# Kernel optimization log

Hardware: AMD Instinct MI355X
Metric: run time of the kernel (lower is better)

Reference implementation:

```python
import jax, jax.numpy as jnp
import numpy as np

N = 50000
E = 800000
G = 16  # graphs in batch
NEG_SLOPE = 0.2


def gatv2_layer(x, src, dst, Wl, bl, Wr, br, att, bias, concat):
    # PyG GATv2Conv: x_j = lin_l(x)[src], x_i = lin_r(x)[dst]
    H, C = att.shape
    n = x.shape[0]
    xl = (x @ Wl + bl).reshape(n, H, C)  # source transform
    xr = (x @ Wr + br).reshape(n, H, C)  # target transform
    e = jax.nn.leaky_relu(xl[src] + xr[dst], NEG_SLOPE)  # [E,H,C]
    score = jnp.einsum('ehc,hc->eh', e, att)             # [E,H]
    # segment softmax over incoming edges of each dst node
    smax = jax.ops.segment_max(score, dst, num_segments=n)   # [n,H]
    ex = jnp.exp(score - smax[dst])
    denom = jax.ops.segment_sum(ex, dst, num_segments=n)
    alpha = ex / (denom[dst] + 1e-16)                        # [E,H]
    out = jax.ops.segment_sum(alpha[:, :, None] * xl[src], dst, num_segments=n)  # [n,H,C]
    if concat:
        return out.reshape(n, H * C) + bias
    return out.mean(axis=1) + bias


def setup_inputs() -> dict:
    key = jax.random.key(0)
    ks = jax.random.split(key, 20)
    x = jax.random.normal(ks[0], (N, 8), dtype=jnp.float32)
    edge_index = jax.random.randint(ks[1], (2, E), 0, N, dtype=jnp.int64)
    batch = jnp.sort(jax.random.randint(ks[2], (N,), 0, G, dtype=jnp.int64))

    def glorot(k, shape):
        lim = np.sqrt(6.0 / (shape[0] + shape[1]))
        return jax.random.uniform(k, shape, jnp.float32, -lim, lim)

    params = dict(
        Wl1=glorot(ks[3], (8, 128)), bl1=jnp.zeros((128,), jnp.float32),
        Wr1=glorot(ks[4], (8, 128)), br1=jnp.zeros((128,), jnp.float32),
        att1=glorot(ks[5], (2, 64)), b1=jnp.zeros((128,), jnp.float32),
        Wl2=glorot(ks[6], (128, 128)), bl2=jnp.zeros((128,), jnp.float32),
        Wr2=glorot(ks[7], (128, 128)), br2=jnp.zeros((128,), jnp.float32),
        att2=glorot(ks[8], (2, 64)), b2=jnp.zeros((128,), jnp.float32),
        Wl3=glorot(ks[9], (128, 32)), bl3=jnp.zeros((32,), jnp.float32),
        Wr3=glorot(ks[10], (128, 32)), br3=jnp.zeros((32,), jnp.float32),
        att3=glorot(ks[11], (1, 32)), b3=jnp.zeros((32,), jnp.float32),
    )
    return dict(x=x, edge_index=edge_index, batch=batch, **params)


def reference(x, edge_index, batch,
              Wl1, bl1, Wr1, br1, att1, b1,
              Wl2, bl2, Wr2, br2, att2, b2,
              Wl3, bl3, Wr3, br3, att3, b3):
    n = x.shape[0]
    loops = jnp.arange(n, dtype=edge_index.dtype)
    src = jnp.concatenate([edge_index[0], loops])  # add_self_loops=True (PyG default)
    dst = jnp.concatenate([edge_index[1], loops])

    h = gatv2_layer(x, src, dst, Wl1, bl1, Wr1, br1, att1, b1, concat=True)
    h = jax.nn.elu(h)
    # dropout(p=0.5) is identity in eval mode
    h = gatv2_layer(h, src, dst, Wl2, bl2, Wr2, br2, att2, b2, concat=True)
    h = jax.nn.elu(h)
    h = gatv2_layer(h, src, dst, Wl3, bl3, Wr3, br3, att3, b3, concat=False)
    h = jax.nn.elu(h)  # [n,32]

    counts = jax.ops.segment_sum(jnp.ones((n,), h.dtype), batch, num_segments=G)
    pooled_mean = jax.ops.segment_sum(h, batch, num_segments=G) / counts[:, None]
    pooled_max = jax.ops.segment_max(h, batch, num_segments=G)
    return jnp.concatenate([pooled_mean, pooled_max], axis=1)  # [G,64]
```

## Files before the change

kernel.cpp:

```cpp
#include <hip/hip_runtime.h>
#include <hip/hip_bf16.h>
#include <math.h>


__device__ __forceinline__ float lrelu(float x) { return x > 0.f ? x : 0.2f * x; }
__device__ __forceinline__ float elu1(float x) { return x > 0.f ? x : expm1f(x); }

__device__ __forceinline__ unsigned f2ord(float x) {
    unsigned b = __float_as_uint(x);
    return (b & 0x80000000u) ? ~b : (b | 0x80000000u);
}
__device__ __forceinline__ float ord2f(unsigned u) {
    unsigned b = (u & 0x80000000u) ? (u & 0x7FFFFFFFu) : ~u;
    return __uint_as_float(b);
}
__device__ __forceinline__ unsigned short f2bf(float f) {
    unsigned u = __float_as_uint(f);
    unsigned r = u + 0x7FFFu + ((u >> 16) & 1u);
    return (unsigned short)(r >> 16);
}

__global__ void k_zero_i32(int* __restrict__ p, int n) {
    int i = blockIdx.x * blockDim.x + threadIdx.x;
    if (i < n) p[i] = 0;
}

__global__ void k_hist(const int* __restrict__ ei, int E, int N, int* __restrict__ deg) {
    int e = blockIdx.x * blockDim.x + threadIdx.x;
    int Etot = E + N;
    if (e >= Etot) return;
    int d = (e < E) ? ei[E + e] : (e - E);
    atomicAdd(&deg[d], 1);
}

__global__ void __launch_bounds__(1024) k_scan(const int* __restrict__ deg, int n,
                                               int* __restrict__ row_off, int* __restrict__ cursor) {
    __shared__ int wsum[16];
    __shared__ int sbase;
    int tid = threadIdx.x;
    int lane = tid & 63, w = tid >> 6;
    if (tid == 0) sbase = 0;
    __syncthreads();
    for (int start = 0; start < n; start += 1024) {
        int i = start + tid;
        int v = (i < n) ? deg[i] : 0;
        int s = v;
        #pragma unroll
        for (int d = 1; d < 64; d <<= 1) {
            int t = __shfl_up(s, d, 64);
            if (lane >= d) s += t;
        }
        if (lane == 63) wsum[w] = s;
        __syncthreads();
        int wbase = 0;
        for (int k = 0; k < w; k++) wbase += wsum[k];
        int excl = sbase + wbase + (s - v);
        if (i < n) { row_off[i] = excl; cursor[i] = excl; }
        __syncthreads();
        if (tid == 1023) sbase = excl + v;
        __syncthreads();
    }
    if (tid == 0) row_off[n] = sbase;
}

__global__ void k_scatter(const int* __restrict__ ei, int E, int N,
                          int* __restrict__ cursor,
                          int* __restrict__ csr_src) {
    int e = blockIdx.x * blockDim.x + threadIdx.x;
    int Etot = E + N;
    if (e >= Etot) return;
    int s, d;
    if (e < E) { s = ei[e]; d = ei[E + e]; } else { s = e - E; d = e - E; }
    int p = atomicAdd(&cursor[d], 1);
    csr_src[p] = s;
}

template <int K>
__global__ void k_linear2b(const float* __restrict__ x, int N,
                           const float* __restrict__ Wl, const float* __restrict__ bl,
                           const float* __restrict__ Wr, const float* __restrict__ br,
                           unsigned short* __restrict__ xlb, float* __restrict__ xr) {
    constexpr int MH = 128, NCG = 64;
    __shared__ float xs[32 * K];
    int tid = threadIdx.x;
    int node0 = blockIdx.x * 32;
    for (int idx = tid * 4; idx < 32 * K; idx += NCG * 4 * 4) {
        int node = node0 + idx / K;
        float4 v = make_float4(0.f, 0.f, 0.f, 0.f);
        if (node < N) v = *(const float4*)(x + (size_t)node0 * K + idx);
        *(float4*)(xs + idx) = v;
    }
    __syncthreads();

    int cg = tid % NCG;
    int ng = tid / NCG;
    bool rightSide = cg >= (MH / 4);
    int c = (rightSide ? cg - MH / 4 : cg) * 4;
    const float* W  = rightSide ? Wr : Wl;
    const float* bb = rightSide ? br : bl;

    float acc[8][4];
    #pragma unroll
    for (int i = 0; i < 8; i++)
        #pragma unroll
        for (int j = 0; j < 4; j++) acc[i][j] = 0.f;

    const float* xrow = xs + ng * 8 * K;
    for (int k0 = 0; k0 < K; k0 += 4) {
        float4 wv[4];
        #pragma unroll
        for (int kk = 0; kk < 4; kk++)
            wv[kk] = *(const float4*)(W + (size_t)(k0 + kk) * MH + c);
        #pragma unroll
        for (int i = 0; i < 8; i++) {
            float4 xv = *(const float4*)(xrow + i * K + k0);
            float xvk[4] = {xv.x, xv.y, xv.z, xv.w};
            #pragma unroll
            for (int kk = 0; kk < 4; kk++) {
                acc[i][0] += xvk[kk] * wv[kk].x;
                acc[i][1] += xvk[kk] * wv[kk].y;
                acc[i][2] += xvk[kk] * wv[kk].z;
                acc[i][3] += xvk[kk] * wv[kk].w;
            }
        }
    }
    float4 bv = *(const float4*)(bb + c);
    #pragma unroll
    for (int i = 0; i < 8; i++) {
        int node = node0 + ng * 8 + i;
        if (node >= N) continue;
        float o0 = acc[i][0] + bv.x, o1 = acc[i][1] + bv.y;
        float o2 = acc[i][2] + bv.z, o3 = acc[i][3] + bv.w;
        if (rightSide) {
            *(float4*)(xr + (size_t)node * MH + c) = make_float4(o0, o1, o2, o3);
        } else {
            ushort4 ub = make_ushort4(f2bf(o0), f2bf(o1), f2bf(o2), f2bf(o3));
            *(ushort4*)(xlb + (size_t)node * MH + c) = ub;
        }
    }
}

__global__ void __launch_bounds__(256) k_linear3(
        const float* __restrict__ x, int N,
        const float* __restrict__ Wl, const float* __restrict__ bl,
        const float* __restrict__ Wr, const float* __restrict__ br,
        float* __restrict__ xl, float* __restrict__ xr) {
    __shared__ float xs[32 * 128];
    int tid = threadIdx.x;
    int node0 = blockIdx.x * 32;
    for (int idx = tid * 4; idx < 32 * 128; idx += 256 * 4) {
        int node = node0 + idx / 128;
        float4 v = make_float4(0.f, 0.f, 0.f, 0.f);
        if (node < N) v = *(const float4*)(x + (size_t)node0 * 128 + idx);
        *(float4*)(xs + idx) = v;
    }
    __syncthreads();
    int cg = tid & 15, ng = tid >> 4;
    bool rightSide = cg >= 8;
    int c = (rightSide ? cg - 8 : cg) * 4;
    const float* W  = rightSide ? Wr : Wl;
    const float* bb = rightSide ? br : bl;
    float* out      = rightSide ? xr : xl;

    float acc[2][4];
    #pragma unroll
    for (int i = 0; i < 2; i++)
        #pragma unroll
        for (int j = 0; j < 4; j++) acc[i][j] = 0.f;

    const float* xrow = xs + ng * 2 * 128;
    for (int k0 = 0; k0 < 128; k0 += 4) {
        float4 wv[4];
        #pragma unroll
        for (int kk = 0; kk < 4; kk++)
            wv[kk] = *(const float4*)(W + (size_t)(k0 + kk) * 32 + c);
        #pragma unroll
        for (int i = 0; i < 2; i++) {
            float4 xv = *(const float4*)(xrow + i * 128 + k0);
            float xvk[4] = {xv.x, xv.y, xv.z, xv.w};
            #pragma unroll
            for (int kk = 0; kk < 4; kk++) {
                acc[i][0] += xvk[kk] * wv[kk].x;
                acc[i][1] += xvk[kk] * wv[kk].y;
                acc[i][2] += xvk[kk] * wv[kk].z;
                acc[i][3] += xvk[kk] * wv[kk].w;
            }
        }
    }
    float4 bv = *(const float4*)(bb + c);
    #pragma unroll
    for (int i = 0; i < 2; i++) {
        int node = node0 + ng * 2 + i;
        if (node < N) {
            float4 o = make_float4(acc[i][0] + bv.x, acc[i][1] + bv.y,
                                   acc[i][2] + bv.z, acc[i][3] + bv.w);
            *(float4*)(out + (size_t)node * 32 + c) = o;
        }
    }
}

__global__ void k_fusedb(const int* __restrict__ row_off, const int* __restrict__ csr_src,
                         const unsigned short* __restrict__ xlb, const float* __restrict__ xr,
                         const float* __restrict__ att, const float* __restrict__ bias,
                         float* __restrict__ hout, int N) {
    constexpr int HC = 128, CPL = 8, GROUP = 8;
    int wid = (blockIdx.x * blockDim.x + threadIdx.x) >> 6;
    int lane = threadIdx.x & 63;
    if (wid >= N) return;
    int slot = lane >> 4;
    int j = lane & 15;
    int c0 = j * CPL;

    int p0 = row_off[wid], p1 = row_off[wid + 1];

    float xrv[CPL], attv[CPL];
    {
        float4 a = *(const float4*)(xr + (size_t)wid * HC + c0);
        float4 b = *(const float4*)(xr + (size_t)wid * HC + c0 + 4);
        xrv[0] = a.x; xrv[1] = a.y; xrv[2] = a.z; xrv[3] = a.w;
        xrv[4] = b.x; xrv[5] = b.y; xrv[6] = b.z; xrv[7] = b.w;
        float4 c = *(const float4*)(att + c0);
        float4 d = *(const float4*)(att + c0 + 4);
        attv[0] = c.x; attv[1] = c.y; attv[2] = c.z; attv[3] = c.w;
        attv[4] = d.x; attv[5] = d.y; attv[6] = d.z; attv[7] = d.w;
    }

    float m = -INFINITY, den = 0.f;
    float acc[CPL];
    #pragma unroll
    for (int q = 0; q < CPL; q++) acc[q] = 0.f;

    int p = p0 + slot;
    int s = (p < p1) ? csr_src[p] : 0;
    while (p < p1) {
        int pn = p + 4;
        int sn = (pn < p1) ? csr_src[pn] : 0;
        int4 rv = *(const int4*)(xlb + (size_t)s * HC + c0);
        float xlv[CPL];
        {
            unsigned u0 = (unsigned)rv.x, u1 = (unsigned)rv.y;
            unsigned u2 = (unsigned)rv.z, u3 = (unsigned)rv.w;
            xlv[0] = __uint_as_float(u0 << 16); xlv[1] = __uint_as_float(u0 & 0xFFFF0000u);
            xlv[2] = __uint_as_float(u1 << 16); xlv[3] = __uint_as_float(u1 & 0xFFFF0000u);
            xlv[4] = __uint_as_float(u2 << 16); xlv[5] = __uint_as_float(u2 & 0xFFFF0000u);
            xlv[6] = __uint_as_float(u3 << 16); xlv[7] = __uint_as_float(u3 & 0xFFFF0000u);
        }
        float part = 0.f;
        #pragma unroll
        for (int q = 0; q < CPL; q++) {
            float t = xlv[q] + xrv[q];
            part = fmaf(fmaxf(t, 0.2f * t), attv[q], part);
        }
        #pragma unroll
        for (int msk = 1; msk < GROUP; msk <<= 1) part += __shfl_xor(part, msk, 64);
        if (part > m + 8.f) {
            float corr = __expf(m - part);
            den *= corr;
            #pragma unroll
            for (int q = 0; q < CPL; q++) acc[q] *= corr;
            m = part;
        }
        float ex = __expf(part - m);
        den += ex;
        #pragma unroll
        for (int q = 0; q < CPL; q++) acc[q] = fmaf(ex, xlv[q], acc[q]);
        p = pn; s = sn;
    }
    float mAll = fmaxf(m, __shfl_xor(m, 16, 64));
    mAll = fmaxf(mAll, __shfl_xor(mAll, 32, 64));
    float scale = __expf(m - mAll);
    float dtot = den * scale;
    dtot += __shfl_xor(dtot, 16, 64);
    dtot += __shfl_xor(dtot, 32, 64);
    #pragma unroll
    for (int q = 0; q < CPL; q++) {
        float a = acc[q] * scale;
        a += __shfl_xor(a, 16, 64);
        a += __shfl_xor(a, 32, 64);
        acc[q] = a;
    }
    if (slot == 0) {
        float inv = 1.0f / (dtot + 1e-16f);
        #pragma unroll
        for (int q = 0; q < CPL; q++) {
            float v = acc[q] * inv + bias[c0 + q];
            hout[(size_t)wid * HC + c0 + q] = elu1(v);
        }
    }
}

template <int CPL>
__device__ __forceinline__ void loadrow(const float* __restrict__ p, float* v) {
    if constexpr (CPL == 8) {
        float4 a = ((const float4*)p)[0];
        float4 b = ((const float4*)p)[1];
        v[0] = a.x; v[1] = a.y; v[2] = a.z; v[3] = a.w;
        v[4] = b.x; v[5] = b.y; v[6] = b.z; v[7] = b.w;
    } else {
        float2 a = ((const float2*)p)[0];
        v[0] = a.x; v[1] = a.y;
    }
}

template <int HC, int C>
__global__ void k_fused(const int* __restrict__ row_off, const int* __restrict__ csr_src,
                        const float* __restrict__ xl, const float* __restrict__ xr,
                        const float* __restrict__ att, const float* __restrict__ bias,
                        float* __restrict__ hout, int N) {
    constexpr int CPL = HC / 16;
    constexpr int GROUP = (16 * C) / HC;
    int wid = (blockIdx.x * blockDim.x + threadIdx.x) >> 6;
    int lane = threadIdx.x & 63;
    if (wid >= N) return;
    int slot = lane >> 4;
    int j = lane & 15;
    int c0 = j * CPL;

    int p0 = row_off[wid], p1 = row_off[wid + 1];

    float xrv[CPL], attv[CPL];
    loadrow<CPL>(xr + (size_t)wid * HC + c0, xrv);
    loadrow<CPL>(att + c0, attv);

    float m = -INFINITY, den = 0.f;
    float acc[CPL];
    #pragma unroll
    for (int q = 0; q < CPL; q++) acc[q] = 0.f;

    int p = p0 + slot;
    int s = (p < p1) ? csr_src[p] : 0;
    while (p < p1) {
        int pn = p + 4;
        int sn = (pn < p1) ? csr_src[pn] : 0;
        float xlv[CPL];
        loadrow<CPL>(xl + (size_t)s * HC + c0, xlv);
        float part = 0.f;
        #pragma unroll
        for (int q = 0; q < CPL; q++) {
            float t = xlv[q] + xrv[q];
            part = fmaf(fmaxf(t, 0.2f * t), attv[q], part);
        }
        #pragma unroll
        for (int msk = 1; msk < GROUP; msk <<= 1) part += __shfl_xor(part, msk, 64);
        if (part > m + 8.f) {
            float corr = __expf(m - part);
            den *= corr;
            #pragma unroll
            for (int q = 0; q < CPL; q++) acc[q] *= corr;
            m = part;
        }
        float ex = __expf(part - m);
        den += ex;
        #pragma unroll
        for (int q = 0; q < CPL; q++) acc[q] = fmaf(ex, xlv[q], acc[q]);
        p = pn; s = sn;
    }
    float mAll = fmaxf(m, __shfl_xor(m, 16, 64));
    mAll = fmaxf(mAll, __shfl_xor(mAll, 32, 64));
    float scale = __expf(m - mAll);
    float dtot = den * scale;
    dtot += __shfl_xor(dtot, 16, 64);
    dtot += __shfl_xor(dtot, 32, 64);
    #pragma unroll
    for (int q = 0; q < CPL; q++) {
        float a = acc[q] * scale;
        a += __shfl_xor(a, 16, 64);
        a += __shfl_xor(a, 32, 64);
        acc[q] = a;
    }
    if (slot == 0) {
        float inv = 1.0f / (dtot + 1e-16f);
        #pragma unroll
        for (int q = 0; q < CPL; q++) {
            float v = acc[q] * inv + bias[c0 + q];
            hout[(size_t)wid * HC + c0 + q] = elu1(v);
        }
    }
}

__global__ void __launch_bounds__(256) k_pool_partial(
        const float* __restrict__ h, const int* __restrict__ batch, int N, int G,
        float* __restrict__ gsum, unsigned* __restrict__ gmax) {
    __shared__ float lsum[512];
    __shared__ unsigned lmax[512];
    int tid = threadIdx.x;
    for (int i = tid; i < G * 32; i += 256) { lsum[i] = 0.f; lmax[i] = 0u; }
    __syncthreads();
    int chunk = (N + gridDim.x - 1) / gridDim.x;
    int start = blockIdx.x * chunk;
    int end = min(N, start + chunk);
    int col = tid & 31, row = tid >> 5;
    int gc = -1; float ps = 0.f; unsigned pm = 0u;
    for (int i = start + row; i < end; i += 8) {
        int g = batch[i];
        if (g != gc) {
            if (gc >= 0) { atomicAdd(&lsum[gc * 32 + col], ps); atomicMax(&lmax[gc * 32 + col], pm); }
            gc = g; ps = 0.f; pm = 0u;
        }
        float v = h[(size_t)i * 32 + col];
        ps += v; pm = max(pm, f2ord(v));
    }
    if (gc >= 0) { atomicAdd(&lsum[gc * 32 + col], ps); atomicMax(&lmax[gc * 32 + col], pm); }
    __syncthreads();
    for (int i = tid; i < G * 32; i += 256) {
        if (lmax[i]) {
            atomicAdd(&gsum[i], lsum[i]);
            atomicMax(&gmax[i], lmax[i]);
        }
    }
}

__global__ void k_pool_final(const float* __restrict__ gsum, const unsigned* __restrict__ gmax,
                             const int* __restrict__ batch, int N, float* __restrict__ out) {
    int g = blockIdx.x;
    int t = threadIdx.x;
    __shared__ int s_cnt;
    if (t == 0) {
        int lo = 0, hi = N;
        while (lo < hi) { int m = (lo + hi) >> 1; if (batch[m] < g) lo = m + 1; else hi = m; }
        int a = lo;
        lo = a; hi = N;
        while (lo < hi) { int m = (lo + hi) >> 1; if (batch[m] < g + 1) lo = m + 1; else hi = m; }
        s_cnt = lo - a;
    }
    __syncthreads();
    if (t < 32) {
        out[g * 64 + t] = gsum[g * 32 + t] / (float)max(s_cnt, 1);
    } else {
        out[g * 64 + t] = ord2f(gmax[g * 32 + (t - 32)]);
    }
}

extern "C" void kernel_launch(void* const* d_in, const int* in_sizes, int n_in,
                              void* d_out, int out_size, void* d_ws, size_t ws_size,
                              hipStream_t stream) {
    const float* x      = (const float*)d_in[0];
    const int*   ei     = (const int*)d_in[1];
    const int*   batch  = (const int*)d_in[2];
    const float* Wl1 = (const float*)d_in[3],  *bl1 = (const float*)d_in[4];
    const float* Wr1 = (const float*)d_in[5],  *br1 = (const float*)d_in[6];
    const float* att1= (const float*)d_in[7],  *b1  = (const float*)d_in[8];
    const float* Wl2 = (const float*)d_in[9],  *bl2 = (const float*)d_in[10];
    const float* Wr2 = (const float*)d_in[11], *br2 = (const float*)d_in[12];
    const float* att2= (const float*)d_in[13], *b2  = (const float*)d_in[14];
    const float* Wl3 = (const float*)d_in[15], *bl3 = (const float*)d_in[16];
    const float* Wr3 = (const float*)d_in[17], *br3 = (const float*)d_in[18];
    const float* att3= (const float*)d_in[19], *b3  = (const float*)d_in[20];

    int N = in_sizes[0] / 8;
    int E = in_sizes[1] / 2;
    int G = out_size / 64;
    int Etot = E + N;

    char* w = (char*)d_ws;
    auto carve = [&](size_t bytes) {
        void* p = (void*)w;
        w += (bytes + 255) & ~(size_t)255;
        return p;
    };
    int*            deg     = (int*)carve((size_t)N * 4);
    int*            row_off = (int*)carve((size_t)(N + 1) * 4);
    int*            cursor  = (int*)carve((size_t)N * 4);
    int*            csr_src = (int*)carve((size_t)Etot * 4);
    float*          gsum    = (float*)carve((size_t)G * 32 * 4);
    unsigned*       gmax    = (unsigned*)carve((size_t)G * 32 * 4);
    unsigned short* xlb     = (unsigned short*)carve((size_t)N * 128 * 2);
    float*          bufA    = (float*)carve((size_t)N * 128 * 4);
    float*          bufB    = (float*)carve((size_t)N * 128 * 4);
    float*          bufC    = (float*)carve((size_t)N * 128 * 4);
    (void)ws_size; (void)n_in;

    k_zero_i32<<<(N + 255) / 256, 256, 0, stream>>>(deg, N);
    k_zero_i32<<<(2 * G * 32 + 255) / 256, 256, 0, stream>>>((int*)gsum, 2 * G * 32);
    k_hist<<<(Etot + 255) / 256, 256, 0, stream>>>(ei, E, N, deg);
    k_scan<<<1, 1024, 0, stream>>>(deg, N, row_off, cursor);
    k_scatter<<<(Etot + 255) / 256, 256, 0, stream>>>(ei, E, N, cursor, csr_src);

    int grdLin = (N + 31) / 32;
    int grdFused = (N + 3) / 4;

    k_linear2b<8><<<grdLin, 256, 0, stream>>>(x, N, Wl1, bl1, Wr1, br1, xlb, bufB);
    k_fusedb<<<grdFused, 256, 0, stream>>>(row_off, csr_src, xlb, bufB, att1, b1, bufC, N);

    k_linear2b<128><<<grdLin, 256, 0, stream>>>(bufC, N, Wl2, bl2, Wr2, br2, xlb, bufB);
    k_fusedb<<<grdFused, 256, 0, stream>>>(row_off, csr_src, xlb, bufB, att2, b2, bufC, N);

    k_linear3<<<grdLin, 256, 0, stream>>>(bufC, N, Wl3, bl3, Wr3, br3, bufA, bufB);
    k_fused<32, 32><<<grdFused, 256, 0, stream>>>(row_off, csr_src, bufA, bufB, att3, b3, bufC, N);

    k_pool_partial<<<256, 256, 0, stream>>>(bufC, batch, N, G, gsum, gmax);
    k_pool_final<<<G, 64, 0, stream>>>(gsum, gmax, batch, N, (float*)d_out);
}
```

Before: 514.6 us.

## Parallelize CSR prefix scan across blocks and unroll edge loop by two

Replaces the single-block serial prefix scan over node degrees with a three-kernel scan: per-block local scan, a one-wave scan of block sums, and an add pass. The gather loop in the bf16 fused attention kernel now handles two edges per slot per iteration, so two row loads are in flight at once and index prefetch goes two steps ahead. The cost is two extra launches and more registers in the fused kernel, which may reduce occupancy.

Result: faster. 481.3 us (-6.5%).

```diff
diff --git a/kernel.cpp b/kernel.cpp
--- a/kernel.cpp
+++ b/kernel.cpp
@@ -33,34 +33,56 @@
     atomicAdd(&deg[d], 1);
 }
 
-__global__ void __launch_bounds__(1024) k_scan(const int* __restrict__ deg, int n,
-                                               int* __restrict__ row_off, int* __restrict__ cursor) {
+__global__ void __launch_bounds__(1024) k_scan_blk(
+        const int* __restrict__ deg, int n,
+        int* __restrict__ part, int* __restrict__ bsum) {
     __shared__ int wsum[16];
-    __shared__ int sbase;
     int tid = threadIdx.x;
     int lane = tid & 63, w = tid >> 6;
-    if (tid == 0) sbase = 0;
+    int i = blockIdx.x * 1024 + tid;
+    int v = (i < n) ? deg[i] : 0;
+    int s = v;
+    #pragma unroll
+    for (int d = 1; d < 64; d <<= 1) {
+        int t = __shfl_up(s, d, 64);
+        if (lane >= d) s += t;
+    }
+    if (lane == 63) wsum[w] = s;
     __syncthreads();
-    for (int start = 0; start < n; start += 1024) {
-        int i = start + tid;
-        int v = (i < n) ? deg[i] : 0;
+    int wbase = 0;
+    for (int k = 0; k < w; k++) wbase += wsum[k];
+    if (i < n) part[i] = wbase + (s - v);
+    if (tid == 1023) bsum[blockIdx.x] = wbase + s;
+}
+
+__global__ void k_scan_top(const int* __restrict__ bsum, int nb,
+                           int* __restrict__ boff, int* __restrict__ row_off, int n) {
+    int lane = threadIdx.x;
+    int base = 0;
+    for (int st = 0; st < nb; st += 64) {
+        int i = st + lane;
+        int v = (i < nb) ? bsum[i] : 0;
         int s = v;
         #pragma unroll
         for (int d = 1; d < 64; d <<= 1) {
             int t = __shfl_up(s, d, 64);
             if (lane >= d) s += t;
         }
-        if (lane == 63) wsum[w] = s;
-        __syncthreads();
-        int wbase = 0;
-        for (int k = 0; k < w; k++) wbase += wsum[k];
-        int excl = sbase + wbase + (s - v);
-        if (i < n) { row_off[i] = excl; cursor[i] = excl; }
-        __syncthreads();
-        if (tid == 1023) sbase = excl + v;
-        __syncthreads();
-    }
-    if (tid == 0) row_off[n] = sbase;
+        if (i < nb) boff[i] = base + (s - v);
+        base += __shfl(s, 63, 64);
+    }
+    if (lane == 0) row_off[n] = base;
+}
+
+__global__ void __launch_bounds__(1024) k_scan_add(
+        const int* __restrict__ part, const int* __restrict__ boff, int n,
+        int* __restrict__ row_off, int* __restrict__ cursor) {
+    int i = blockIdx.x * 1024 + threadIdx.x;
+    if (i < n) {
+        int r = part[i] + boff[blockIdx.x];
+        row_off[i] = r;
+        cursor[i] = r;
+    }
 }
 
 __global__ void k_scatter(const int* __restrict__ ei, int E, int N,
@@ -199,6 +221,15 @@
     }
 }
 
+__device__ __forceinline__ void unpack8(int4 rv, float* v) {
+    unsigned u0 = (unsigned)rv.x, u1 = (unsigned)rv.y;
+    unsigned u2 = (unsigned)rv.z, u3 = (unsigned)rv.w;
+    v[0] = __uint_as_float(u0 << 16); v[1] = __uint_as_float(u0 & 0xFFFF0000u);
+    v[2] = __uint_as_float(u1 << 16); v[3] = __uint_as_float(u1 & 0xFFFF0000u);
+    v[4] = __uint_as_float(u2 << 16); v[5] = __uint_as_float(u2 & 0xFFFF0000u);
+    v[6] = __uint_as_float(u3 << 16); v[7] = __uint_as_float(u3 & 0xFFFF0000u);
+}
+
 __global__ void k_fusedb(const int* __restrict__ row_off, const int* __restrict__ csr_src,
                          const unsigned short* __restrict__ xlb, const float* __restrict__ xr,
                          const float* __restrict__ att, const float* __restrict__ bias,
@@ -231,40 +262,56 @@
     for (int q = 0; q < CPL; q++) acc[q] = 0.f;
 
     int p = p0 + slot;
-    int s = (p < p1) ? csr_src[p] : 0;
+    int s0 = (p < p1) ? csr_src[p] : 0;
+    int s1 = (p + 4 < p1) ? csr_src[p + 4] : 0;
     while (p < p1) {
-        int pn = p + 4;
-        int sn = (pn < p1) ? csr_src[pn] : 0;
-        int4 rv = *(const int4*)(xlb + (size_t)s * HC + c0);
-        float xlv[CPL];
-        {
-            unsigned u0 = (unsigned)rv.x, u1 = (unsigned)rv.y;
-            unsigned u2 = (unsigned)rv.z, u3 = (unsigned)rv.w;
-            xlv[0] = __uint_as_float(u0 << 16); xlv[1] = __uint_as_float(u0 & 0xFFFF0000u);
-            xlv[2] = __uint_as_float(u1 << 16); xlv[3] = __uint_as_float(u1 & 0xFFFF0000u);
-            xlv[4] = __uint_as_float(u2 << 16); xlv[5] = __uint_as_float(u2 & 0xFFFF0000u);
-            xlv[6] = __uint_as_float(u3 << 16); xlv[7] = __uint_as_float(u3 & 0xFFFF0000u);
-        }
-        float part = 0.f;
+        int np = p + 8;
+        int ns0 = (np < p1) ? csr_src[np] : 0;
+        int ns1 = (np + 4 < p1) ? csr_src[np + 4] : 0;
+        bool has2 = (p + 4) < p1;
+        int4 ra = *(const int4*)(xlb + (size_t)s0 * HC + c0);
+        int4 rb = *(const int4*)(xlb + (size_t)s1 * HC + c0);
+        float xa[CPL], xb[CPL];
+        unpack8(ra, xa);
+        unpack8(rb, xb);
+        float pa = 0.f, pb = 0.f;
         #pragma unroll
         for (int q = 0; q < CPL; q++) {
-            float t = xlv[q] + xrv[q];
-            part = fmaf(fmaxf(t, 0.2f * t), attv[q], part);
-        }
-        #pragma unroll
-        for (int msk = 1; msk < GROUP; msk <<= 1) part += __shfl_xor(part, msk, 64);
-        if (part > m + 8.f) {
-            float corr = __expf(m - part);
+            float ta = xa[q] + xrv[q];
+            float tb = xb[q] + xrv[q];
+            pa = fmaf(fmaxf(ta, 0.2f * ta), attv[q], pa);
+            pb = fmaf(fmaxf(tb, 0.2f * tb), attv[q], pb);
+        }
+        #pragma unroll
+        for (int msk = 1; msk < GROUP; msk <<= 1) {
+            pa += __shfl_xor(pa, msk, 64);
+            pb += __shfl_xor(pb, msk, 64);
+        }
+        if (pa > m + 8.f) {
+            float corr = __expf(m - pa);
             den *= corr;
             #pragma unroll
             for (int q = 0; q < CPL; q++) acc[q] *= corr;
-            m = part;
-        }
-        float ex = __expf(part - m);
-        den += ex;
-        #pragma unroll
-        for (int q = 0; q < CPL; q++) acc[q] = fmaf(ex, xlv[q], acc[q]);
-        p = pn; s = sn;
+            m = pa;
+        }
+        float ea = __expf(pa - m);
+        den += ea;
+        #pragma unroll
+        for (int q = 0; q < CPL; q++) acc[q] = fmaf(ea, xa[q], acc[q]);
+        if (has2) {
+            if (pb > m + 8.f) {
+                float corr = __expf(m - pb);
+                den *= corr;
+                #pragma unroll
+                for (int q = 0; q < CPL; q++) acc[q] *= corr;
+                m = pb;
+            }
+            float eb = __expf(pb - m);
+            den += eb;
+            #pragma unroll
+            for (int q = 0; q < CPL; q++) acc[q] = fmaf(eb, xb[q], acc[q]);
+        }
+        p = np; s0 = ns0; s1 = ns1;
     }
     float mAll = fmaxf(m, __shfl_xor(m, 16, 64));
     mAll = fmaxf(mAll, __shfl_xor(mAll, 32, 64));
@@ -451,6 +498,7 @@
     int E = in_sizes[1] / 2;
     int G = out_size / 64;
     int Etot = E + N;
+    int nb = (N + 1023) / 1024;
 
     char* w = (char*)d_ws;
     auto carve = [&](size_t bytes) {
@@ -461,6 +509,9 @@
     int*            deg     = (int*)carve((size_t)N * 4);
     int*            row_off = (int*)carve((size_t)(N + 1) * 4);
     int*            cursor  = (int*)carve((size_t)N * 4);
+    int*            part    = (int*)carve((size_t)N * 4);
+    int*            bsum    = (int*)carve((size_t)nb * 4);
+    int*            boff    = (int*)carve((size_t)nb * 4);
     int*            csr_src = (int*)carve((size_t)Etot * 4);
     float*          gsum    = (float*)carve((size_t)G * 32 * 4);
     unsigned*       gmax    = (unsigned*)carve((size_t)G * 32 * 4);
@@ -473,7 +524,9 @@
     k_zero_i32<<<(N + 255) / 256, 256, 0, stream>>>(deg, N);
     k_zero_i32<<<(2 * G * 32 + 255) / 256, 256, 0, stream>>>((int*)gsum, 2 * G * 32);
     k_hist<<<(Etot + 255) / 256, 256, 0, stream>>>(ei, E, N, deg);
-    k_scan<<<1, 1024, 0, stream>>>(deg, N, row_off, cursor);
+    k_scan_blk<<<nb, 1024, 0, stream>>>(deg, N, part, bsum);
+    k_scan_top<<<1, 64, 0, stream>>>(bsum, nb, boff, row_off, N);
+    k_scan_add<<<nb, 1024, 0, stream>>>(part, boff, N, row_off, cursor);
     k_scatter<<<(Etot + 255) / 256, 256, 0, stream>>>(ei, E, N, cursor, csr_src);
 
     int grdLin = (N + 31) / 32;
```
